# Kernel optimization log

Hardware: AMD Instinct MI355X
Metric: run time of the kernel (lower is better)

The kernel has to match this reference:

```python
import jax, jax.numpy as jnp
import numpy as np

N, F, C, H, E, G, L = 50000, 128, 64, 4, 500000, 32, 4
EPS = 1e-5
NEG_SLOPE = 0.2


def setup_inputs() -> dict:
    key = jax.random.key(0)
    ks = jax.random.split(key, 16)
    x = jax.random.normal(ks[0], (N, F), dtype=jnp.float32)
    edge_index = jax.random.randint(ks[1], (2, E), 0, N, dtype=jnp.int64)
    batch = jnp.sort(jax.random.randint(ks[2], (N,), 0, G, dtype=jnp.int64))
    s = 0.05
    params = {
        'Wp': jax.random.normal(ks[3], (F, C), jnp.float32) * s,          # initial_proj (no bias)
        'Wl': jax.random.normal(ks[4], (L, C, H * C), jnp.float32) * s,   # GATv2 lin_l per layer
        'bl': jax.random.normal(ks[5], (L, H * C), jnp.float32) * s,
        'Wr': jax.random.normal(ks[6], (L, C, H * C), jnp.float32) * s,   # GATv2 lin_r per layer
        'br': jax.random.normal(ks[7], (L, H * C), jnp.float32) * s,
        'att': jax.random.normal(ks[8], (L, H, C), jnp.float32) * s,      # attention vector per head
        'cb': jax.random.normal(ks[9], (L, C), jnp.float32) * s,          # conv output bias (concat=False)
        'ln_w': jnp.ones((L, C), jnp.float32),                            # pyg LayerNorm affine
        'ln_b': jnp.zeros((L, C), jnp.float32),
        'Wh': jax.random.normal(ks[10], (C, 1), jnp.float32) * s,         # head
        'bh': jnp.zeros((1,), jnp.float32),
    }
    return {'x': x, 'edge_index': edge_index, 'batch': batch, **params}


def _gatv2(x, src, dst, Wl, bl, Wr, br, att, cb):
    # x: [N, C] -> per-head projections [N, H, C]
    xl = (x @ Wl + bl).reshape(N, H, C)
    xr = (x @ Wr + br).reshape(N, H, C)
    # edge-wise GATv2 scores: leaky_relu(x_i + x_j) . att   -> [E, H]
    e = jax.nn.leaky_relu(xl[src] + xr[dst], NEG_SLOPE)
    score = jnp.einsum('ehc,hc->eh', e, att)
    # segment softmax over incoming edges of each destination node
    m = jax.ops.segment_max(score, dst, num_segments=N)[dst]
    p = jnp.exp(score - m)
    denom = jax.ops.segment_sum(p, dst, num_segments=N)[dst]
    alpha = p / denom                                     # [E, H]
    msg = xl[src] * alpha[..., None]                      # [E, H, C]
    out = jax.ops.segment_sum(msg, dst, num_segments=N)   # [N, H, C]
    return out.mean(axis=1) + cb                          # concat=False: head mean + bias


def _graph_norm(x, w, b):
    # pyg.nn.LayerNorm mode='graph' with batch=None: normalize over ALL elements
    xc = x - x.mean()
    std = jnp.sqrt(xc.var())
    return (xc / (std + EPS)) * w + b


def reference(x, edge_index, batch, Wp, Wl, bl, Wr, br, att, cb, ln_w, ln_b, Wh, bh):
    src, dst = edge_index[0], edge_index[1]
    h = x @ Wp
    for l in range(L):
        h = _gatv2(h, src, dst, Wl[l], bl[l], Wr[l], br[l], att[l], cb[l])
        h = jax.nn.selu(_graph_norm(h, ln_w[l], ln_b[l]))
    # global mean pool over graphs
    counts = jax.ops.segment_sum(jnp.ones((N,), h.dtype), batch, num_segments=G)
    pooled = jax.ops.segment_sum(h, batch, num_segments=G) / jnp.maximum(counts, 1.0)[:, None]
    return (pooled @ Wh + bh).squeeze(-1)  # [G]
```

## Files before the change

### kernel.cpp

```cpp
#include <hip/hip_runtime.h>
#include <hip/hip_bf16.h>
#include <hip/hip_fp8.h>
#include <math.h>

#define NN 50000
#define FIN 128
#define CC 64
#define HH 4
#define HC 256
#define EE 500000
#define GG 32
#define LL 4

typedef __hip_bfloat16 bf16;
typedef __attribute__((ext_vector_type(2))) float f2;
typedef __attribute__((ext_vector_type(8))) short s8v;
typedef __attribute__((ext_vector_type(4))) float f4v;

__device__ __forceinline__ float b2f(bf16 v){ return __bfloat162float(v); }
__device__ __forceinline__ bf16 f2b(float v){ return __float2bfloat16(v); }
__device__ __forceinline__ void unpack2(unsigned u, float& a, float& b){
  union { unsigned q; float f; } x, y;
  x.q = u << 16; y.q = u & 0xffff0000u; a = x.f; b = y.f;
}
__device__ __forceinline__ f2 unpackf2(unsigned u){
  union { unsigned q; float f; } x, y;
  x.q = u << 16; y.q = u & 0xffff0000u;
  f2 r; r.x = x.f; r.y = y.f; return r;
}
__device__ __forceinline__ f2 maxf2(f2 a, f2 b){
#if __has_builtin(__builtin_elementwise_max)
  return __builtin_elementwise_max(a, b);
#else
  f2 r; r.x = fmaxf(a.x, b.x); r.y = fmaxf(a.y, b.y); return r;
#endif
}
__device__ __forceinline__ float clamp4(float v){ return fminf(fmaxf(v, -1e4f), 1e4f); }
__device__ __forceinline__ unsigned pack2bf(float a, float b){
  bf16 x = f2b(clamp4(a)), y = f2b(clamp4(b));
  unsigned short ux = *(unsigned short*)&x, uy = *(unsigned short*)&y;
  return (unsigned)ux | ((unsigned)uy << 16);
}
__device__ __forceinline__ unsigned f4_to_fp8x4(float a, float b, float c, float d){
  a = fminf(fmaxf(a, -240.f), 240.f);
  b = fminf(fmaxf(b, -240.f), 240.f);
  c = fminf(fmaxf(c, -240.f), 240.f);
  d = fminf(fmaxf(d, -240.f), 240.f);
#if __has_builtin(__builtin_amdgcn_cvt_pk_fp8_f32)
  int p = 0;
  p = __builtin_amdgcn_cvt_pk_fp8_f32(a, b, p, false);
  p = __builtin_amdgcn_cvt_pk_fp8_f32(c, d, p, true);
  return (unsigned)p;
#else
  __hip_fp8_e4m3 qa(a), qb(b), qc(c), qd(d);
  return (unsigned)qa.__x | ((unsigned)qb.__x << 8) | ((unsigned)qc.__x << 16) | ((unsigned)qd.__x << 24);
#endif
}
__device__ __forceinline__ void fp8x4_to_f2(unsigned u, f2& lo, f2& hi){
#if __has_builtin(__builtin_amdgcn_cvt_pk_f32_fp8)
  lo = __builtin_amdgcn_cvt_pk_f32_fp8((int)u, false);
  hi = __builtin_amdgcn_cvt_pk_f32_fp8((int)u, true);
#else
  __hip_fp8_e4m3 q0, q1, q2, q3;
  q0.__x = u & 0xff; q1.__x = (u >> 8) & 0xff; q2.__x = (u >> 16) & 0xff; q3.__x = (u >> 24) & 0xff;
  lo.x = (float)q0; lo.y = (float)q1; hi.x = (float)q2; hi.y = (float)q3;
#endif
}
__device__ __forceinline__ float selu_f(float y){
  const float SS = 1.0507009873554805f, SA = 1.6732632423543772f;
  return y > 0.f ? SS*y : SS*SA*(__expf(y) - 1.f);
}
__device__ __forceinline__ int ld_i(const void* p, int i, int w8){
  if (w8) return (int)((const long long*)p)[i];
  return ((const int*)p)[i];
}
__device__ __forceinline__ void stats_inline(const float* __restrict__ partials, float& mu, float& inv){
  float s1 = 0.f, s2 = 0.f;
  #pragma unroll 8
  for (int i = 0; i < 64; ++i){ s1 += partials[i]; s2 += partials[64 + i]; }
  float cnt = (float)NN * 64.f;
  mu = s1 / cnt;
  float var = s2 / cnt - mu*mu;
  if (!(var > 0.f)) var = 0.f;
  inv = 1.0f / (sqrtf(var) + 1e-5f);
}

__global__ __launch_bounds__(256) void k_setup(
    const void* ei, const void* batch,
    const void* Wp, const void* Wl, const void* bl, const void* Wr, const void* br,
    const void* att, const void* cb, const void* lnw, const void* lnb,
    const void* Wh, const void* bh,
    float* dst, int* deg, float* pooled, int* flags, short* apack){
  int b = blockIdx.x;
  int t = threadIdx.x;
  const unsigned short* lw = (const unsigned short*)lnw;
  int f32 = (lw[0] == 0x0000 && lw[1] == 0x3F80) ? 1 : 0;
  if (b < 560){
    int i = b*256 + t;
    if (i < 143169){
      const void* src; int idx;
      if      (i < 8192)   { src = Wp;  idx = i; }
      else if (i < 73728)  { src = Wl;  idx = i - 8192; }
      else if (i < 74752)  { src = bl;  idx = i - 73728; }
      else if (i < 140288) { src = Wr;  idx = i - 74752; }
      else if (i < 141312) { src = br;  idx = i - 140288; }
      else if (i < 142336) { src = att; idx = i - 141312; }
      else if (i < 142592) { src = cb;  idx = i - 142336; }
      else if (i < 142848) { src = lnw; idx = i - 142592; }
      else if (i < 143104) { src = lnb; idx = i - 142848; }
      else if (i < 143168) { src = Wh;  idx = i - 143104; }
      else                 { src = bh;  idx = 0; }
      dst[i] = f32 ? ((const float*)src)[idx] : b2f(((const bf16*)src)[idx]);
    }
  } else if (b < 756){
    int i = (b - 560)*256 + t;
    if (i < NN) deg[i] = 0;
  } else if (b == 756){
    for (int i = t; i < GG*64; i += 256) pooled[i] = 0.f;
    if (t < 64){
      int lane = t;
      const int* w  = (const int*)ei;
      const int* wb = (const int*)batch;
      int bad_e = (lane < 32) ? (w[2*(lane*15625) + 1] != 0) : 0;
      int bad_b = (lane < 32) ? (wb[25001 + 2*lane] != 0) : 0;
      unsigned long long me = __ballot(bad_e);
      unsigned long long mb = __ballot(bad_b);
      if (lane == 0){
        flags[0] = (me == 0ULL) ? 1 : 0;
        flags[1] = (mb == 0ULL) ? 1 : 0;
        flags[2] = f32;
      }
    }
  } else {
    int i2 = (b - 757)*256 + t;
    int l   = i2 >> 15;
    int rem = i2 & 32767;
    int ct  = rem >> 10;
    int rem2 = rem & 1023;
    int kh  = rem2 >> 9;
    int li  = (rem2 >> 3) & 63;
    int j   = rem2 & 7;
    int k   = kh*32 + ((li >> 4) << 3) + j;
    int c   = (ct << 4) + (li & 15);
    const void* Wsrc = (c < 256) ? Wl : Wr;
    int cc = c & 255;
    size_t idx = ((size_t)l*64 + k)*256 + cc;
    float v = f32 ? ((const float*)Wsrc)[idx] : b2f(((const bf16*)Wsrc)[idx]);
    bf16 bv = f2b(v);
    apack[i2] = *(short*)&bv;
  }
}

__global__ __launch_bounds__(256) void k_hist(const void* __restrict__ ei, int* __restrict__ deg,
                                              const int* __restrict__ flags){
  int e = blockIdx.x*256 + threadIdx.x;
  if (e < EE){
    int d = ld_i(ei, EE + e, flags[0]);
    if ((unsigned)d < NN) atomicAdd(&deg[d], 1);
  }
}

__global__ __launch_bounds__(256) void k_scan1(const int* __restrict__ deg, int* __restrict__ off,
                                               int* __restrict__ btot){
  int t = threadIdx.x;
  int i = blockIdx.x*256 + t;
  int v = (i < NN) ? deg[i] : 0;
  int incl = v;
  #pragma unroll
  for (int dl = 1; dl < 64; dl <<= 1){
    int u = __shfl_up(incl, dl, 64);
    if ((t & 63) >= dl) incl += u;
  }
  __shared__ int wt[4];
  if ((t & 63) == 63) wt[t >> 6] = incl;
  __syncthreads();
  int base = 0;
  for (int ww = 0; ww < (t >> 6); ++ww) base += wt[ww];
  incl += base;
  if (i < NN) off[i + 1] = incl;
  if (t == 255) btot[blockIdx.x] = incl;
}

__global__ __launch_bounds__(256) void k_scan2(const int* __restrict__ btot, int* __restrict__ boff, int nb){
  int t = threadIdx.x;
  int v = (t < nb) ? btot[t] : 0;
  int incl = v;
  #pragma unroll
  for (int dl = 1; dl < 64; dl <<= 1){
    int u = __shfl_up(incl, dl, 64);
    if ((t & 63) >= dl) incl += u;
  }
  __shared__ int wt[4];
  if ((t & 63) == 63) wt[t >> 6] = incl;
  __syncthreads();
  int base = 0;
  for (int ww = 0; ww < (t >> 6); ++ww) base += wt[ww];
  incl += base;
  if (t < 256) boff[t] = incl - v;
}

__global__ __launch_bounds__(256) void k_scan3(int* __restrict__ off, int* __restrict__ cursor,
                                               const int* __restrict__ deg, const int* __restrict__ boff){
  int i = blockIdx.x*256 + threadIdx.x;
  if (i >= NN) return;
  int v = off[i + 1] + boff[i >> 8];
  off[i + 1] = v;
  cursor[i] = v - deg[i];
  if (i == 0) off[0] = 0;
}

__global__ __launch_bounds__(256) void k_scatter_gb(const void* __restrict__ ei, int* __restrict__ cursor,
                                                    int* __restrict__ ssrc, const void* __restrict__ batch,
                                                    int* __restrict__ gstart, const int* __restrict__ flags){
  int b = blockIdx.x;
  if (b < 1954){
    int e = b*256 + threadIdx.x;
    if (e < EE){
      int f = flags[0];
      int s = ld_i(ei, e, f);
      int d = ld_i(ei, EE + e, f);
      if ((unsigned)d < NN && (unsigned)s < NN){
        int p = atomicAdd(&cursor[d], 1);
        ssrc[p] = s << 8;
      }
    }
  } else {
    int i = (b - 1954)*256 + threadIdx.x;
    if (i >= NN) return;
    int f = flags[1];
    int bb = ld_i(batch, i, f);
    bb = min(max(bb, 0), GG - 1);
    if (i == 0){ for (int q = 0; q <= bb; ++q) gstart[q] = 0; }
    else {
      int pb = ld_i(batch, i - 1, f);
      pb = min(max(pb, 0), GG - 1);
      for (int q = pb + 1; q <= bb; ++q) gstart[q] = i;
    }
    if (i == NN - 1){ for (int q = bb + 1; q <= GG; ++q) gstart[q] = NN; }
  }
}

__global__ __launch_bounds__(256) void k_proj(const void* __restrict__ xraw, const float* __restrict__ Wp32,
                                              float* __restrict__ h, const int* __restrict__ flags){
  __shared__ float xs[64*128];
  __shared__ float wsm[128*64];
  int t = threadIdx.x;
  int r0 = blockIdx.x * 64;
  int rows = NN - r0; if (rows > 64) rows = 64;
  const float4* gw = (const float4*)Wp32;
  #pragma unroll
  for (int i = 0; i < 8; ++i) ((float4*)wsm)[i*256 + t] = gw[i*256 + t];
  int f32 = flags[2];
  #pragma unroll
  for (int i = 0; i < 8; ++i){
    int p = i*256 + t;
    int r = p >> 5, kq = p & 31;
    float4 v = make_float4(0.f,0.f,0.f,0.f);
    if (r < rows){
      if (f32) v = ((const float4*)xraw)[(size_t)(r0 + r)*32 + kq];
      else {
        uint2 u = ((const uint2*)xraw)[(size_t)(r0 + r)*32 + kq];
        unpack2(u.x, v.x, v.y); unpack2(u.y, v.z, v.w);
      }
    }
    *(float4*)&xs[r*128 + kq*4] = v;
  }
  __syncthreads();
  int tx = t & 15, ty = t >> 4;
  int c0 = tx*4, rr0 = ty*4;
  float acc[4][4] = {{0.f}};
  for (int k = 0; k < 128; k += 4){
    float4 xv[4];
    #pragma unroll
    for (int i = 0; i < 4; ++i) xv[i] = *(const float4*)&xs[(rr0 + i)*128 + k];
    const float* xf = (const float*)xv;
    #pragma unroll
    for (int m = 0; m < 4; ++m){
      float4 wv = *(const float4*)&wsm[(k + m)*64 + c0];
      #pragma unroll
      for (int i = 0; i < 4; ++i){
        float xm = xf[i*4 + m];
        acc[i][0] = fmaf(xm, wv.x, acc[i][0]);
        acc[i][1] = fmaf(xm, wv.y, acc[i][1]);
        acc[i][2] = fmaf(xm, wv.z, acc[i][2]);
        acc[i][3] = fmaf(xm, wv.w, acc[i][3]);
      }
    }
  }
  #pragma unroll
  for (int i = 0; i < 4; ++i){
    int r = rr0 + i;
    if (r < rows){
      float4 o;
      o.x = clamp4(acc[i][0]); o.y = clamp4(acc[i][1]);
      o.z = clamp4(acc[i][2]); o.w = clamp4(acc[i][3]);
      *(float4*)&h[(size_t)(r0 + r)*64 + c0] = o;
    }
  }
}

__global__ __launch_bounds__(256) void k_gemm2m(const float* __restrict__ h,
    const s8v* __restrict__ apack,
    const float* __restrict__ bl, const float* __restrict__ br,
    unsigned char* __restrict__ xl8, bf16* __restrict__ xr,
    const float* __restrict__ partials, const float* __restrict__ lnw, const float* __restrict__ lnb,
    int apply){
  __shared__ short buf[64*264];
  int t = threadIdx.x;
  int r0 = blockIdx.x * 64;
  int rows = NN - r0; if (rows > 64) rows = 64;
  float mu = 0.f, inv = 0.f;
  if (apply) stats_inline(partials, mu, inv);
  #pragma unroll
  for (int i = 0; i < 4; ++i){
    int p = i*256 + t;
    int r = p >> 4, kq = p & 15;
    uint2 pk; pk.x = 0u; pk.y = 0u;
    if (r < rows){
      float4 v = ((const float4*)h)[(size_t)(r0 + r)*16 + kq];
      if (apply){
        float4 w4 = *(const float4*)(lnw + kq*4);
        float4 b4 = *(const float4*)(lnb + kq*4);
        v.x = selu_f((v.x - mu)*inv*w4.x + b4.x);
        v.y = selu_f((v.y - mu)*inv*w4.y + b4.y);
        v.z = selu_f((v.z - mu)*inv*w4.z + b4.z);
        v.w = selu_f((v.w - mu)*inv*w4.w + b4.w);
      }
      pk.x = pack2bf(v.x, v.y);
      pk.y = pack2bf(v.z, v.w);
    }
    *(uint2*)&buf[r*264 + kq*4] = pk;
  }
  __syncthreads();
  int wave = t >> 6, lane = t & 63;
  int n = lane & 15, q = lane >> 4;
  int rowb = wave * 16;
  s8v bf0 = *(const s8v*)&buf[(rowb + n)*264 + q*8];
  s8v bf1 = *(const s8v*)&buf[(rowb + n)*264 + 32 + q*8];
  __syncthreads();
  {
    unsigned* ubuf = (unsigned*)buf;
    #pragma unroll 4
    for (int cc = 0; cc < 16; ++cc){
      s8v a0 = apack[cc*128 + lane];
      s8v a1 = apack[cc*128 + 64 + lane];
      f4v acc = {0.f, 0.f, 0.f, 0.f};
      acc = __builtin_amdgcn_mfma_f32_16x16x32_bf16(a0, bf0, acc, 0, 0, 0);
      acc = __builtin_amdgcn_mfma_f32_16x16x32_bf16(a1, bf1, acc, 0, 0, 0);
      int colh = (cc << 4) + (q << 2);
      float4 bb = *(const float4*)&bl[colh];
      ubuf[(rowb + n)*132 + (colh >> 2)] =
          f4_to_fp8x4(acc[0] + bb.x, acc[1] + bb.y, acc[2] + bb.z, acc[3] + bb.w);
    }
    __syncthreads();
    #pragma unroll
    for (int i = 0; i < 16; ++i){
      int idx = i*256 + t;
      int row = idx >> 6, colu = idx & 63;
      if (row < rows){
        unsigned v = ubuf[row*132 + colu];
        ((unsigned*)xl8)[((size_t)(r0 + row))*64 + colu] = v;
      }
    }
    __syncthreads();
  }
  {
    #pragma unroll 4
    for (int cc = 0; cc < 16; ++cc){
      int ct = 16 + cc;
      s8v a0 = apack[ct*128 + lane];
      s8v a1 = apack[ct*128 + 64 + lane];
      f4v acc = {0.f, 0.f, 0.f, 0.f};
      acc = __builtin_amdgcn_mfma_f32_16x16x32_bf16(a0, bf0, acc, 0, 0, 0);
      acc = __builtin_amdgcn_mfma_f32_16x16x32_bf16(a1, bf1, acc, 0, 0, 0);
      int colh = (cc << 4) + (q << 2);
      float4 bb = *(const float4*)&br[colh];
      uint2 pk;
      pk.x = pack2bf(acc[0] + bb.x, acc[1] + bb.y);
      pk.y = pack2bf(acc[2] + bb.z, acc[3] + bb.w);
      *(uint2*)&buf[(rowb + n)*264 + colh] = pk;
    }
    __syncthreads();
    #pragma unroll
    for (int i = 0; i < 16; ++i){
      int idx = i*256 + t;
      int row = idx >> 6, col = idx & 63;
      if (row < rows){
        uint2 v = *(const uint2*)&buf[row*264 + col*4];
        *(uint2*)&xr[((size_t)(r0 + row))*256 + col*4] = v;
      }
    }
  }
}

__global__ __launch_bounds__(256) void k_gat(const unsigned char* __restrict__ xl8, const bf16* __restrict__ xr,
    const int* __restrict__ off, const int* __restrict__ ssrc,
    const float* __restrict__ att, const float* __restrict__ cbp,
    float* __restrict__ out, float2* __restrict__ nstat){
  int t = threadIdx.x;
  int wave = t >> 6, lane = t & 63;
  int d = blockIdx.x*4 + wave;
  if (d >= NN) return;
  int s0 = off[d], s1 = off[d + 1];
  int head = lane >> 4;
  int c4 = (lane & 15) * 4;

  float4 av4 = *(const float4*)(att + head*64 + c4);
  f2 av01; av01.x = av4.x; av01.y = av4.y;
  f2 av23; av23.x = av4.z; av23.y = av4.w;
  uint2 ur = *(const uint2*)(xr + (size_t)d * 256 + lane*4);
  f2 r01 = unpackf2(ur.x), r23 = unpackf2(ur.y);
  const float NS = 0.2f;

  float denom = 0.f;
  f2 m01; m01.x = 0.f; m01.y = 0.f;
  f2 m23; m23.x = 0.f; m23.y = 0.f;
  int e = s0;
  for (; e + 1 < s1; e += 2){
    int ofa = ssrc[e];
    int ofb = ssrc[e + 1];
    unsigned ua = *(const unsigned*)(xl8 + (size_t)(unsigned)ofa + lane*4);
    unsigned ub = *(const unsigned*)(xl8 + (size_t)(unsigned)ofb + lane*4);
    f2 xa01, xa23, xb01, xb23;
    fp8x4_to_f2(ua, xa01, xa23);
    fp8x4_to_f2(ub, xb01, xb23);
    f2 ta01 = xa01 + r01, ta23 = xa23 + r23;
    f2 tb01 = xb01 + r01, tb23 = xb23 + r23;
    ta01 = maxf2(ta01, ta01*NS); ta23 = maxf2(ta23, ta23*NS);
    tb01 = maxf2(tb01, tb01*NS); tb23 = maxf2(tb23, tb23*NS);
    f2 sa2 = av01*ta01 + av23*ta23;
    f2 sb2 = av01*tb01 + av23*tb23;
    float sa = sa2.x + sa2.y;
    float sb = sb2.x + sb2.y;
    sa += __shfl_xor(sa, 1, 64); sb += __shfl_xor(sb, 1, 64);
    sa += __shfl_xor(sa, 2, 64); sb += __shfl_xor(sb, 2, 64);
    sa += __shfl_xor(sa, 4, 64); sb += __shfl_xor(sb, 4, 64);
    sa += __shfl_xor(sa, 8, 64); sb += __shfl_xor(sb, 8, 64);
    float pa = __expf(fminf(sa, 30.f));
    float pb = __expf(fminf(sb, 30.f));
    denom += pa + pb;
    m01 = m01 + xa01*pa + xb01*pb;
    m23 = m23 + xa23*pa + xb23*pb;
  }
  if (e < s1){
    int ofa = ssrc[e];
    unsigned ua = *(const unsigned*)(xl8 + (size_t)(unsigned)ofa + lane*4);
    f2 xa01, xa23;
    fp8x4_to_f2(ua, xa01, xa23);
    f2 ta01 = xa01 + r01, ta23 = xa23 + r23;
    ta01 = maxf2(ta01, ta01*NS); ta23 = maxf2(ta23, ta23*NS);
    f2 sa2 = av01*ta01 + av23*ta23;
    float sa = sa2.x + sa2.y;
    sa += __shfl_xor(sa, 1, 64); sa += __shfl_xor(sa, 2, 64);
    sa += __shfl_xor(sa, 4, 64); sa += __shfl_xor(sa, 8, 64);
    float pa = __expf(fminf(sa, 30.f));
    denom += pa;
    m01 = m01 + xa01*pa;
    m23 = m23 + xa23*pa;
  }
  float inv = denom > 0.f ? 1.0f / denom : 0.f;
  float v0 = m01.x*inv, v1 = m01.y*inv, v2 = m23.x*inv, v3 = m23.y*inv;
  v0 += __shfl_xor(v0, 16, 64); v1 += __shfl_xor(v1, 16, 64);
  v2 += __shfl_xor(v2, 16, 64); v3 += __shfl_xor(v3, 16, 64);
  v0 += __shfl_xor(v0, 32, 64); v1 += __shfl_xor(v1, 32, 64);
  v2 += __shfl_xor(v2, 32, 64); v3 += __shfl_xor(v3, 32, 64);
  if (lane < 16){
    float4 cbv = *(const float4*)(cbp + c4);
    float4 o;
    o.x = clamp4(0.25f*v0 + cbv.x); o.y = clamp4(0.25f*v1 + cbv.y);
    o.z = clamp4(0.25f*v2 + cbv.z); o.w = clamp4(0.25f*v3 + cbv.w);
    ((float4*)(out + (size_t)d * 64))[lane] = o;
    float s1p = o.x + o.y + o.z + o.w;
    float s2p = o.x*o.x + o.y*o.y + o.z*o.z + o.w*o.w;
    s1p += __shfl_xor(s1p, 1, 64); s2p += __shfl_xor(s2p, 1, 64);
    s1p += __shfl_xor(s1p, 2, 64); s2p += __shfl_xor(s2p, 2, 64);
    s1p += __shfl_xor(s1p, 4, 64); s2p += __shfl_xor(s2p, 4, 64);
    s1p += __shfl_xor(s1p, 8, 64); s2p += __shfl_xor(s2p, 8, 64);
    if (lane == 0){
      float2 ns; ns.x = s1p; ns.y = s2p;
      nstat[d] = ns;
    }
  }
}

__global__ __launch_bounds__(256) void k_nstat(const float2* __restrict__ nstat, float* __restrict__ partials){
  int t = threadIdx.x;
  int gid = blockIdx.x*256 + t;
  float s1 = 0.f, s2 = 0.f;
  for (int i = gid; i < NN; i += 64*256){
    float2 v = nstat[i];
    s1 += v.x; s2 += v.y;
  }
  #pragma unroll
  for (int dl = 1; dl < 64; dl <<= 1){ s1 += __shfl_xor(s1, dl, 64); s2 += __shfl_xor(s2, dl, 64); }
  __shared__ float l1[4], l2[4];
  int w = t >> 6;
  if ((t & 63) == 0){ l1[w] = s1; l2[w] = s2; }
  __syncthreads();
  if (t == 0){
    partials[blockIdx.x]      = l1[0] + l1[1] + l1[2] + l1[3];
    partials[64 + blockIdx.x] = l2[0] + l2[1] + l2[2] + l2[3];
  }
}

__global__ __launch_bounds__(256) void k_poolA(const float* __restrict__ h, const void* __restrict__ batch,
                                               float* __restrict__ pooled, const int* __restrict__ flags,
                                               const float* __restrict__ partials,
                                               const float* __restrict__ lnw, const float* __restrict__ lnb){
  int t = threadIdx.x;
  int c = t & 63, rq = t >> 6;
  int r0 = blockIdx.x * 256;
  int r1 = r0 + 256; if (r1 > NN) r1 = NN;
  int f = flags[1];
  float mu, inv;
  stats_inline(partials, mu, inv);
  float wc = lnw[c], bc = lnb[c];
  float acc = 0.f;
  int cur_g = -1;
  for (int r = r0 + rq; r < r1; r += 4){
    int g = ld_i(batch, r, f);
    g = min(max(g, 0), GG - 1);
    if (g != cur_g){
      if (cur_g >= 0) atomicAdd(&pooled[cur_g*64 + c], acc);
      acc = 0.f; cur_g = g;
    }
    acc += selu_f((h[(size_t)r*64 + c] - mu)*inv*wc + bc);
  }
  if (cur_g >= 0) atomicAdd(&pooled[cur_g*64 + c], acc);
}

__global__ __launch_bounds__(64) void k_poolB(const float* __restrict__ pooled, const int* __restrict__ gstart,
    const float* __restrict__ Wh, const float* __restrict__ bh, void* __restrict__ outp,
    const int* __restrict__ flags){
  int g = blockIdx.x, t = threadIdx.x;
  int rs = gstart[g], re = gstart[g + 1];
  int cnt = re - rs; if (cnt < 1) cnt = 1;
  float val = (pooled[g*64 + t] / (float)cnt) * Wh[t];
  #pragma unroll
  for (int dl = 1; dl < 64; dl <<= 1) val += __shfl_xor(val, dl, 64);
  if (t == 0){
    float res = val + bh[0];
    if (flags[2]) ((float*)outp)[g] = res;
    else          ((bf16*)outp)[g] = f2b(res);
  }
}

extern "C" void kernel_launch(void* const* d_in, const int* in_sizes, int n_in,
                              void* d_out, int out_size, void* d_ws, size_t ws_size,
                              hipStream_t stream) {
  const void* x     = d_in[0];
  const void* ei    = d_in[1];
  const void* batch = d_in[2];
  const void* Wp    = d_in[3];
  const void* Wl    = d_in[4];
  const void* bl    = d_in[5];
  const void* Wr    = d_in[6];
  const void* br    = d_in[7];
  const void* att   = d_in[8];
  const void* cb    = d_in[9];
  const void* lnw   = d_in[10];
  const void* lnb   = d_in[11];
  const void* Wh    = d_in[12];
  const void* bh    = d_in[13];

  char* w = (char*)d_ws;
  int*   flags  = (int*)w;     w += 256;
  int*   deg    = (int*)w;     w += 200192;
  int*   off    = (int*)w;     w += 200192;
  int*   cursor = (int*)w;     w += 200192;
  int*   btot   = (int*)w;     w += 1024;
  int*   boff   = (int*)w;     w += 1024;
  int*   gstart = (int*)w;     w += 256;
  float* partials = (float*)w; w += 2048;
  float* pooled = (float*)w;   w += GG*64*4;
  float* wcvt   = (float*)w;   w += 572928;
  short* apack  = (short*)w;   w += 262144;
  float2* nstat = (float2*)w;  w += (size_t)NN*8;
  int*   ssrc   = (int*)w;     w += (size_t)EE*4;
  float* hbuf   = (float*)w;   w += (size_t)NN*64*4;
  unsigned char* xlb = (unsigned char*)w; w += (size_t)NN*256;
  bf16*  xrb    = (bf16*)w;    w += (size_t)NN*256*2;

  float* Wp32  = wcvt;
  float* bl32  = wcvt + 73728;
  float* br32  = wcvt + 140288;
  float* att32 = wcvt + 141312;
  float* cb32  = wcvt + 142336;
  float* lnw32 = wcvt + 142592;
  float* lnb32 = wcvt + 142848;
  float* Wh32  = wcvt + 143104;
  float* bh32  = wcvt + 143168;

  const int NB = (NN + 255) / 256;
  const int NT = (NN + 63) / 64;

  k_setup<<<757 + 512, 256, 0, stream>>>(ei, batch, Wp, Wl, bl, Wr, br, att, cb, lnw, lnb, Wh, bh,
                                         wcvt, deg, pooled, flags, apack);
  k_hist<<<(EE + 255)/256, 256, 0, stream>>>(ei, deg, flags);
  k_scan1<<<NB, 256, 0, stream>>>(deg, off, btot);
  k_scan2<<<1, 256, 0, stream>>>(btot, boff, NB);
  k_scan3<<<NB, 256, 0, stream>>>(off, cursor, deg, boff);
  k_scatter_gb<<<1954 + NB, 256, 0, stream>>>(ei, cursor, ssrc, batch, gstart, flags);

  k_proj<<<NT, 256, 0, stream>>>(x, Wp32, hbuf, flags);

  for (int l = 0; l < LL; ++l){
    int lp = (l > 0) ? (l - 1) : 0;
    k_gemm2m<<<NT, 256, 0, stream>>>(hbuf,
        (const s8v*)(apack + (size_t)l*32768),
        bl32 + (size_t)l*256, br32 + (size_t)l*256, xlb, xrb,
        partials, lnw32 + (size_t)lp*CC, lnb32 + (size_t)lp*CC, l > 0 ? 1 : 0);
    k_gat<<<(NN + 3)/4, 256, 0, stream>>>(xlb, xrb, off, ssrc,
        att32 + (size_t)l*HH*CC, cb32 + (size_t)l*CC, hbuf, nstat);
    k_nstat<<<64, 256, 0, stream>>>(nstat, partials);
  }

  k_poolA<<<NB, 256, 0, stream>>>(hbuf, batch, pooled, flags, partials,
      lnw32 + (size_t)3*CC, lnb32 + (size_t)3*CC);
  k_poolB<<<GG, 64, 0, stream>>>(pooled, gstart, Wh32, bh32, d_out, flags);
}
```

Measured before the change: 507.7 us.

## Process four edges per wave concurrently in GAT aggregation kernel

Remaps the per-destination GAT wave so each 16-lane group handles a different incoming edge, with each lane loading 16 fp8 features (uint4) instead of 4. Score reduction needs only two shuffle steps, and partial softmax sums and messages are combined across edge groups at the end. The aim is more memory-level parallelism per wave and fewer serial shuffle chains per edge. The cost is more registers per lane, extra end-of-loop shuffle reductions, and wasted lanes when a node's degree is not a multiple of four (average degree is about ten).

New measurement: 602.6 us. 18.7% more time.

```diff
diff --git a/kernel.cpp b/kernel.cpp
--- a/kernel.cpp
+++ b/kernel.cpp
@@ -402,80 +402,107 @@
   int d = blockIdx.x*4 + wave;
   if (d >= NN) return;
   int s0 = off[d], s1 = off[d + 1];
-  int head = lane >> 4;
-  int c4 = (lane & 15) * 4;
-
-  float4 av4 = *(const float4*)(att + head*64 + c4);
-  f2 av01; av01.x = av4.x; av01.y = av4.y;
-  f2 av23; av23.x = av4.z; av23.y = av4.w;
-  uint2 ur = *(const uint2*)(xr + (size_t)d * 256 + lane*4);
-  f2 r01 = unpackf2(ur.x), r23 = unpackf2(ur.y);
+  int g = lane >> 4;
+  int l4 = lane & 15;
+  int head = l4 >> 2;
+  int chb = (l4 & 3) * 16;
+
+  f2 av[8];
+  {
+    const float* ap = att + head*64 + chb;
+    float4 a0 = *(const float4*)(ap);
+    float4 a1 = *(const float4*)(ap + 4);
+    float4 a2 = *(const float4*)(ap + 8);
+    float4 a3 = *(const float4*)(ap + 12);
+    av[0].x=a0.x; av[0].y=a0.y; av[1].x=a0.z; av[1].y=a0.w;
+    av[2].x=a1.x; av[2].y=a1.y; av[3].x=a1.z; av[3].y=a1.w;
+    av[4].x=a2.x; av[4].y=a2.y; av[5].x=a2.z; av[5].y=a2.w;
+    av[6].x=a3.x; av[6].y=a3.y; av[7].x=a3.z; av[7].y=a3.w;
+  }
+  f2 r[8];
+  {
+    const unsigned short* rp = (const unsigned short*)(xr + (size_t)d*256) + l4*16;
+    uint4 u0 = *(const uint4*)rp;
+    uint4 u1 = *(const uint4*)(rp + 8);
+    r[0] = unpackf2(u0.x); r[1] = unpackf2(u0.y); r[2] = unpackf2(u0.z); r[3] = unpackf2(u0.w);
+    r[4] = unpackf2(u1.x); r[5] = unpackf2(u1.y); r[6] = unpackf2(u1.z); r[7] = unpackf2(u1.w);
+  }
   const float NS = 0.2f;
-
   float denom = 0.f;
-  f2 m01; m01.x = 0.f; m01.y = 0.f;
-  f2 m23; m23.x = 0.f; m23.y = 0.f;
-  int e = s0;
-  for (; e + 1 < s1; e += 2){
-    int ofa = ssrc[e];
-    int ofb = ssrc[e + 1];
-    unsigned ua = *(const unsigned*)(xl8 + (size_t)(unsigned)ofa + lane*4);
-    unsigned ub = *(const unsigned*)(xl8 + (size_t)(unsigned)ofb + lane*4);
-    f2 xa01, xa23, xb01, xb23;
-    fp8x4_to_f2(ua, xa01, xa23);
-    fp8x4_to_f2(ub, xb01, xb23);
-    f2 ta01 = xa01 + r01, ta23 = xa23 + r23;
-    f2 tb01 = xb01 + r01, tb23 = xb23 + r23;
-    ta01 = maxf2(ta01, ta01*NS); ta23 = maxf2(ta23, ta23*NS);
-    tb01 = maxf2(tb01, tb01*NS); tb23 = maxf2(tb23, tb23*NS);
-    f2 sa2 = av01*ta01 + av23*ta23;
-    f2 sb2 = av01*tb01 + av23*tb23;
-    float sa = sa2.x + sa2.y;
-    float sb = sb2.x + sb2.y;
-    sa += __shfl_xor(sa, 1, 64); sb += __shfl_xor(sb, 1, 64);
-    sa += __shfl_xor(sa, 2, 64); sb += __shfl_xor(sb, 2, 64);
-    sa += __shfl_xor(sa, 4, 64); sb += __shfl_xor(sb, 4, 64);
-    sa += __shfl_xor(sa, 8, 64); sb += __shfl_xor(sb, 8, 64);
-    float pa = __expf(fminf(sa, 30.f));
-    float pb = __expf(fminf(sb, 30.f));
-    denom += pa + pb;
-    m01 = m01 + xa01*pa + xb01*pb;
-    m23 = m23 + xa23*pa + xb23*pb;
-  }
-  if (e < s1){
-    int ofa = ssrc[e];
-    unsigned ua = *(const unsigned*)(xl8 + (size_t)(unsigned)ofa + lane*4);
-    f2 xa01, xa23;
-    fp8x4_to_f2(ua, xa01, xa23);
-    f2 ta01 = xa01 + r01, ta23 = xa23 + r23;
-    ta01 = maxf2(ta01, ta01*NS); ta23 = maxf2(ta23, ta23*NS);
-    f2 sa2 = av01*ta01 + av23*ta23;
-    float sa = sa2.x + sa2.y;
-    sa += __shfl_xor(sa, 1, 64); sa += __shfl_xor(sa, 2, 64);
-    sa += __shfl_xor(sa, 4, 64); sa += __shfl_xor(sa, 8, 64);
-    float pa = __expf(fminf(sa, 30.f));
-    denom += pa;
-    m01 = m01 + xa01*pa;
-    m23 = m23 + xa23*pa;
+  f2 m[8];
+  #pragma unroll
+  for (int i = 0; i < 8; ++i){ m[i].x = 0.f; m[i].y = 0.f; }
+
+  for (int e = s0; e < s1; e += 4){
+    int my = e + g;
+    int idx = (my < s1) ? my : (s1 - 1);
+    int ofs = ssrc[idx];
+    uint4 u = *(const uint4*)(xl8 + (size_t)(unsigned)ofs + l4*16);
+    f2 x[8];
+    fp8x4_to_f2(u.x, x[0], x[1]);
+    fp8x4_to_f2(u.y, x[2], x[3]);
+    fp8x4_to_f2(u.z, x[4], x[5]);
+    fp8x4_to_f2(u.w, x[6], x[7]);
+    f2 acc2; acc2.x = 0.f; acc2.y = 0.f;
+    #pragma unroll
+    for (int i = 0; i < 8; ++i){
+      f2 tt = x[i] + r[i];
+      tt = maxf2(tt, tt*NS);
+      acc2 += av[i]*tt;
+    }
+    float sc = acc2.x + acc2.y;
+    sc += __shfl_xor(sc, 1, 64);
+    sc += __shfl_xor(sc, 2, 64);
+    sc = fminf(sc, 30.f);
+    float p = __expf(sc);
+    if (my >= s1) p = 0.f;
+    denom += p;
+    #pragma unroll
+    for (int i = 0; i < 8; ++i) m[i] += x[i]*p;
+  }
+  denom += __shfl_xor(denom, 16, 64);
+  denom += __shfl_xor(denom, 32, 64);
+  #pragma unroll
+  for (int i = 0; i < 8; ++i){
+    m[i].x += __shfl_xor(m[i].x, 16, 64); m[i].y += __shfl_xor(m[i].y, 16, 64);
+    m[i].x += __shfl_xor(m[i].x, 32, 64); m[i].y += __shfl_xor(m[i].y, 32, 64);
   }
   float inv = denom > 0.f ? 1.0f / denom : 0.f;
-  float v0 = m01.x*inv, v1 = m01.y*inv, v2 = m23.x*inv, v3 = m23.y*inv;
-  v0 += __shfl_xor(v0, 16, 64); v1 += __shfl_xor(v1, 16, 64);
-  v2 += __shfl_xor(v2, 16, 64); v3 += __shfl_xor(v3, 16, 64);
-  v0 += __shfl_xor(v0, 32, 64); v1 += __shfl_xor(v1, 32, 64);
-  v2 += __shfl_xor(v2, 32, 64); v3 += __shfl_xor(v3, 32, 64);
-  if (lane < 16){
-    float4 cbv = *(const float4*)(cbp + c4);
-    float4 o;
-    o.x = clamp4(0.25f*v0 + cbv.x); o.y = clamp4(0.25f*v1 + cbv.y);
-    o.z = clamp4(0.25f*v2 + cbv.z); o.w = clamp4(0.25f*v3 + cbv.w);
-    ((float4*)(out + (size_t)d * 64))[lane] = o;
-    float s1p = o.x + o.y + o.z + o.w;
-    float s2p = o.x*o.x + o.y*o.y + o.z*o.z + o.w*o.w;
+  #pragma unroll
+  for (int i = 0; i < 8; ++i){ m[i].x *= inv; m[i].y *= inv; }
+  #pragma unroll
+  for (int i = 0; i < 8; ++i){
+    m[i].x += __shfl_xor(m[i].x, 4, 64); m[i].y += __shfl_xor(m[i].y, 4, 64);
+    m[i].x += __shfl_xor(m[i].x, 8, 64); m[i].y += __shfl_xor(m[i].y, 8, 64);
+  }
+  if (lane < 4){
+    const float* cp = cbp + lane*16;
+    float* op = out + (size_t)d*64 + lane*16;
+    float4 c0 = *(const float4*)(cp);
+    float4 c1 = *(const float4*)(cp + 4);
+    float4 c2 = *(const float4*)(cp + 8);
+    float4 c3 = *(const float4*)(cp + 12);
+    float4 o0, o1, o2, o3;
+    o0.x = clamp4(0.25f*m[0].x + c0.x); o0.y = clamp4(0.25f*m[0].y + c0.y);
+    o0.z = clamp4(0.25f*m[1].x + c0.z); o0.w = clamp4(0.25f*m[1].y + c0.w);
+    o1.x = clamp4(0.25f*m[2].x + c1.x); o1.y = clamp4(0.25f*m[2].y + c1.y);
+    o1.z = clamp4(0.25f*m[3].x + c1.z); o1.w = clamp4(0.25f*m[3].y + c1.w);
+    o2.x = clamp4(0.25f*m[4].x + c2.x); o2.y = clamp4(0.25f*m[4].y + c2.y);
+    o2.z = clamp4(0.25f*m[5].x + c2.z); o2.w = clamp4(0.25f*m[5].y + c2.w);
+    o3.x = clamp4(0.25f*m[6].x + c3.x); o3.y = clamp4(0.25f*m[6].y + c3.y);
+    o3.z = clamp4(0.25f*m[7].x + c3.z); o3.w = clamp4(0.25f*m[7].y + c3.w);
+    *(float4*)(op)      = o0;
+    *(float4*)(op + 4)  = o1;
+    *(float4*)(op + 8)  = o2;
+    *(float4*)(op + 12) = o3;
+    float s1p = o0.x+o0.y+o0.z+o0.w + o1.x+o1.y+o1.z+o1.w
+              + o2.x+o2.y+o2.z+o2.w + o3.x+o3.y+o3.z+o3.w;
+    float s2p = o0.x*o0.x+o0.y*o0.y+o0.z*o0.z+o0.w*o0.w
+              + o1.x*o1.x+o1.y*o1.y+o1.z*o1.z+o1.w*o1.w
+              + o2.x*o2.x+o2.y*o2.y+o2.z*o2.z+o2.w*o2.w
+              + o3.x*o3.x+o3.y*o3.y+o3.z*o3.z+o3.w*o3.w;
     s1p += __shfl_xor(s1p, 1, 64); s2p += __shfl_xor(s2p, 1, 64);
     s1p += __shfl_xor(s1p, 2, 64); s2p += __shfl_xor(s2p, 2, 64);
-    s1p += __shfl_xor(s1p, 4, 64); s2p += __shfl_xor(s2p, 4, 64);
-    s1p += __shfl_xor(s1p, 8, 64); s2p += __shfl_xor(s2p, 8, 64);
     if (lane == 0){
       float2 ns; ns.x = s1p; ns.y = s2p;
       nstat[d] = ns;
```
